# Kernel optimization log

Measured on AMD Instinct MI355X. Metric: run time of the kernel, lower is better.

The kernel has to match this reference:

```python
import jax, jax.numpy as jnp
import numpy as np

# Model dims (match init_kwargs)
M = 4          # bits per symbol
T = 32         # spike-encoding timesteps
F = 41         # input_features (tap window)
H = 256        # hidden_features
O = 16         # output_features
B = 4096       # batch

# LIF parameters (norse LIFParameters as constructed in __init__)
DT = 0.001
ALPHA = 100.0
V_TH = 1.0
V_LEAK = 0.0
V_RESET = 0.0
TAU_MEM_INV = 100.0
TAU_SYN_INV = 200.0


@jax.custom_vjp
def spike(x):
    # norse heaviside with SuperSpike surrogate gradient
    return (x > 0).astype(x.dtype)

def _spike_fwd(x):
    return spike(x), x

def _spike_bwd(x, g):
    return (g / (ALPHA * jnp.abs(x) + 1.0) ** 2,)

spike.defvjp(_spike_fwd, _spike_bwd)


def setup_inputs() -> dict:
    key = jax.random.key(0)
    ks = jax.random.split(key, 6)
    x = jax.random.randint(ks[0], (B, F), 0, 2 ** M)  # symbol indices
    # nn.Embedding default init: N(0,1)
    emb = jax.random.normal(ks[1], (2 ** M, M * T), dtype=jnp.float32)
    # nn.Linear default init: U(-1/sqrt(fan_in), 1/sqrt(fan_in))
    s_in = 1.0 / np.sqrt(M * F)
    W_in = jax.random.uniform(ks[2], (H, M * F), minval=-s_in, maxval=s_in, dtype=jnp.float32)
    W_rec = jax.random.normal(ks[3], (H, H), dtype=jnp.float32) / np.sqrt(H)
    W_rec = W_rec * (1.0 - jnp.eye(H, dtype=jnp.float32))  # autapses=False: zero diagonal
    s_out = 1.0 / np.sqrt(H)
    W_out = jax.random.uniform(ks[4], (O, H), minval=-s_out, maxval=s_out, dtype=jnp.float32)
    b_out = jax.random.uniform(ks[5], (O,), minval=-s_out, maxval=s_out, dtype=jnp.float32)
    return {"x": x, "emb": emb, "W_in": W_in, "W_rec": W_rec, "W_out": W_out, "b_out": b_out}


def reference(x, emb, W_in, W_rec, W_out, b_out):
    b = x.shape[0]
    xe = emb[x]                                      # (B, F, M*T)
    xe = xe.reshape(b, T, M * F).transpose(1, 0, 2)  # (T, B, M*F)

    z0 = jnp.zeros((b, H), jnp.float32)
    v0 = jnp.full((b, H), V_LEAK, jnp.float32)
    i0 = jnp.zeros((b, H), jnp.float32)

    def step(carry, xt):
        z, v, i = carry
        # LIF dynamics (norse lif_step): decay membrane & synaptic current
        v_dec = v + DT * TAU_MEM_INV * ((V_LEAK - v) + i)
        i_dec = i * (1.0 - DT * TAU_SYN_INV)
        z_new = spike(v_dec - V_TH)
        v_new = (1.0 - z_new) * v_dec + z_new * V_RESET
        # new current: feedforward input + recurrence on PREVIOUS spikes
        i_new = i_dec + xt @ W_in.T + z @ W_rec.T
        out_t = z_new @ W_out.T + b_out
        return (z_new, v_new, i_new), (z_new, out_t)

    _, (spikes, outs) = jax.lax.scan(step, (z0, v0, i0), xe)
    spikerate = jnp.sum(spikes) / (T * b * H)
    z_sum = jnp.sum(outs, axis=0)  # decode: sum over timesteps -> (B, O)
    return z_sum, spikerate
```

## Files before the change

kernel.cpp:

```cpp
#include <hip/hip_runtime.h>


#define T_STEPS 32
#define FDIM    41
#define HDIM    256
#define ODIM    16
#define BDIM    4096
#define MF      164

#define P_FLOATS  (32 * 3 * 16 * 256)
#define WT_FLOATS (256 * 256)

__global__ __launch_bounds__(256) void k_prep(const float* __restrict__ emb,
                                              const float* __restrict__ W_in,
                                              const float* __restrict__ W_rec,
                                              float* __restrict__ P,
                                              float* __restrict__ WT,
                                              int* __restrict__ counter)
{
    const int bid = blockIdx.x;
    const int tid = threadIdx.x;

    if (bid < 96) {
        const int t  = bid / 3;
        const int si = bid % 3;
        const int k0   = t * MF;
        const int f    = (k0 >> 7) + si;
        const int base = f << 7;
        const int c0   = max(k0, base) - base;
        const int c1   = min(k0 + MF, base + 128) - base;
        const int len  = c1 - c0;

        if (len <= 0) {
            #pragma unroll
            for (int s = 0; s < 16; ++s)
                P[((t * 3 + si) * 16 + s) * 256 + tid] = 0.0f;
            return;
        }

        __shared__ float emb_lds[16][128];
        for (int idx = tid; idx < 16 * 128; idx += 256) {
            const int s = idx >> 7, u = idx & 127;
            if (u < len) emb_lds[s][u] = emb[(s << 7) + c0 + u];
        }
        __syncthreads();

        const int j0 = base + c0 - k0;
        double acc[16];
        #pragma unroll
        for (int s = 0; s < 16; ++s) acc[s] = 0.0;
        for (int u = 0; u < len; ++u) {
            const double w = (double)W_in[tid * MF + j0 + u];
            #pragma unroll
            for (int s = 0; s < 16; ++s)
                acc[s] += w * (double)emb_lds[s][u];
        }
        #pragma unroll
        for (int s = 0; s < 16; ++s)
            P[((t * 3 + si) * 16 + s) * 256 + tid] = (float)acc[s];
    } else {
        const int h = bid - 96;
        WT[h * 256 + tid] = W_rec[tid * 256 + h];
        if (h == 0 && tid == 0) *counter = 0;
    }
}

__global__ __launch_bounds__(256) void k_main(const int* __restrict__ x,
                                              const float* __restrict__ P,
                                              const float* __restrict__ WT,
                                              const float* __restrict__ W_out,
                                              const float* __restrict__ b_out,
                                              float* __restrict__ out,
                                              int* __restrict__ counter)
{
#pragma clang fp contract(off)
    __shared__ float cnt_lds[4][256];
    __shared__ int   red[4];

    const int tid  = threadIdx.x;
    const int lane = tid & 63;
    const int wv   = __builtin_amdgcn_readfirstlane(tid >> 6);
    const int b    = blockIdx.x * 4 + wv;

    const int*    __restrict__ xb  = x + b * FDIM;
    const float4* __restrict__ P4  = (const float4*)P;
    const float4* __restrict__ WT4 = (const float4*)WT;

    int sym[FDIM];
    #pragma unroll
    for (int f = 0; f < FDIM; ++f)
        sym[f] = __builtin_amdgcn_readfirstlane(xb[f]);

    float vx = 0.f, vy = 0.f, vz = 0.f, vw = 0.f;
    float ix = 0.f, iy = 0.f, iz = 0.f, iw = 0.f;
    int   n0 = 0, n1 = 0, n2 = 0, n3 = 0;
    unsigned long long m0 = 0, m1 = 0, m2 = 0, m3 = 0;

    float4 pf[4][3];

    #define ISSUE(T, SLOT)                                                   \
        do {                                                                 \
            const int f0_ = ((T) * MF) >> 7;                                 \
            const int f2_ = (f0_ + 2 < FDIM) ? f0_ + 2 : FDIM - 1;           \
            pf[SLOT][0] = P4[(((T) * 3 + 0) * 16 + sym[f0_]) * 64 + lane];   \
            pf[SLOT][1] = P4[(((T) * 3 + 1) * 16 + sym[f0_ + 1]) * 64 + lane];\
            pf[SLOT][2] = P4[(((T) * 3 + 2) * 16 + sym[f2_]) * 64 + lane];   \
        } while (0)

    #pragma unroll
    for (int t = 0; t < 4; ++t) ISSUE(t, t);

    #pragma unroll
    for (int t = 0; t < T_STEPS; ++t) {
        const int slot = t & 3;

        const float4 p0 = pf[slot][0];
        const float4 p1 = pf[slot][1];
        const float4 p2 = pf[slot][2];

        if (t + 4 < T_STEPS) ISSUE(t + 4, slot);

        const float fx = (p0.x + p1.x) + p2.x;
        const float fy = (p0.y + p1.y) + p2.y;
        const float fz = (p0.z + p1.z) + p2.z;
        const float fw = (p0.w + p1.w) + p2.w;

        float rx = 0.f, ry = 0.f, rz = 0.f, rw = 0.f;
        while (m0) {
            const int l = __builtin_ctzll(m0); m0 &= m0 - 1;
            const float4 w = WT4[(4 * l + 0) * 64 + lane];
            rx += w.x; ry += w.y; rz += w.z; rw += w.w;
        }
        while (m1) {
            const int l = __builtin_ctzll(m1); m1 &= m1 - 1;
            const float4 w = WT4[(4 * l + 1) * 64 + lane];
            rx += w.x; ry += w.y; rz += w.z; rw += w.w;
        }
        while (m2) {
            const int l = __builtin_ctzll(m2); m2 &= m2 - 1;
            const float4 w = WT4[(4 * l + 2) * 64 + lane];
            rx += w.x; ry += w.y; rz += w.z; rw += w.w;
        }
        while (m3) {
            const int l = __builtin_ctzll(m3); m3 &= m3 - 1;
            const float4 w = WT4[(4 * l + 3) * 64 + lane];
            rx += w.x; ry += w.y; rz += w.z; rw += w.w;
        }

        const float vdx = vx + 0.1f * (ix - vx);
        const float vdy = vy + 0.1f * (iy - vy);
        const float vdz = vz + 0.1f * (iz - vz);
        const float vdw = vw + 0.1f * (iw - vw);
        const float idx_ = ix * 0.8f;
        const float idy_ = iy * 0.8f;
        const float idz_ = iz * 0.8f;
        const float idw_ = iw * 0.8f;

        const bool z0 = vdx > 1.0f;
        const bool z1 = vdy > 1.0f;
        const bool z2 = vdz > 1.0f;
        const bool z3 = vdw > 1.0f;

        vx = z0 ? 0.0f : vdx;
        vy = z1 ? 0.0f : vdy;
        vz = z2 ? 0.0f : vdz;
        vw = z3 ? 0.0f : vdw;

        ix = (idx_ + fx) + rx;
        iy = (idy_ + fy) + ry;
        iz = (idz_ + fz) + rz;
        iw = (idw_ + fw) + rw;

        n0 += z0; n1 += z1; n2 += z2; n3 += z3;

        m0 = __ballot(z0);
        m1 = __ballot(z1);
        m2 = __ballot(z2);
        m3 = __ballot(z3);
    }
    #undef ISSUE

    cnt_lds[wv][4 * lane + 0] = (float)n0;
    cnt_lds[wv][4 * lane + 1] = (float)n1;
    cnt_lds[wv][4 * lane + 2] = (float)n2;
    cnt_lds[wv][4 * lane + 3] = (float)n3;

    int myspk = n0 + n1 + n2 + n3;
    #pragma unroll
    for (int off = 32; off > 0; off >>= 1)
        myspk += __shfl_down(myspk, off, 64);
    if (lane == 0) red[wv] = myspk;

    __syncthreads();
    if (tid == 0) atomicAdd(counter, red[0] + red[1] + red[2] + red[3]);

    {
        const int o = lane & 15;
        const int q = lane >> 4;
        const float* __restrict__ wo = W_out + o * 256 + q * 64;
        const float* __restrict__ cl = cnt_lds[wv] + q * 64;
        float acc = 0.0f;
        #pragma unroll 8
        for (int h = 0; h < 64; ++h)
            acc += cl[h] * wo[h];
        acc += __shfl_down(acc, 16, 64);
        acc += __shfl_down(acc, 32, 64);
        if (q == 0)
            out[b * ODIM + o] = 32.0f * b_out[o] + acc;
    }
}

__global__ void k_fin(const int* __restrict__ counter, float* __restrict__ out)
{
    out[BDIM * ODIM] = (float)(*counter) * (1.0f / 33554432.0f);
}

extern "C" void kernel_launch(void* const* d_in, const int* in_sizes, int n_in,
                              void* d_out, int out_size, void* d_ws, size_t ws_size,
                              hipStream_t stream)
{
    const int*   x     = (const int*)  d_in[0];
    const float* emb   = (const float*)d_in[1];
    const float* W_in  = (const float*)d_in[2];
    const float* W_rec = (const float*)d_in[3];
    const float* W_out = (const float*)d_in[4];
    const float* b_out = (const float*)d_in[5];
    float* out = (float*)d_out;

    float* P       = (float*)d_ws;
    float* WT      = P + P_FLOATS;
    int*   counter = (int*)(WT + WT_FLOATS);

    k_prep<<<96 + 256, 256, 0, stream>>>(emb, W_in, W_rec, P, WT, counter);
    k_main<<<BDIM / 4, 256, 0, stream>>>(x, P, WT, W_out, b_out, out, counter);
    k_fin<<<1, 1, 0, stream>>>(counter, out);
}
```

Before: 59.12 us.

## Compact spike indices in LDS and prefetch recurrent weight rows one step ahead

The serial ctz loop over ballot masks is replaced by a compaction step: each wave writes the indices of spiking neurons into an LDS list using mbcnt prefix counts. The recurrent weight rows for up to 12 spikes are then issued as batched loads one timestep before they are needed, using A/B double-buffered register sets, and a zero-padded sentinel row in WT keeps the groups of four uniform. The aim is to overlap the dependent global loads with the LIF update and to remove the serialized load-then-add chain. The cost is much higher register pressure from the 24 float4 buffers plus extra LDS traffic, and any spikes beyond 12 still fall back to an in-step loop.

```diff
diff --git a/kernel.cpp b/kernel.cpp
--- a/kernel.cpp
+++ b/kernel.cpp
@@ -1,15 +1,23 @@
 #include <hip/hip_runtime.h>
 
+
+typedef float f32x4 __attribute__((ext_vector_type(4)));
+typedef int   i32x4 __attribute__((ext_vector_type(4)));
 
 #define T_STEPS 32
 #define FDIM    41
-#define HDIM    256
 #define ODIM    16
 #define BDIM    4096
 #define MF      164
 
 #define P_FLOATS  (32 * 3 * 16 * 256)
-#define WT_FLOATS (256 * 256)
+#define WT_ROWS   257
+#define WT_FLOATS (WT_ROWS * 256)
+
+__device__ __forceinline__ unsigned mbcnt64(unsigned long long m) {
+    unsigned lo = __builtin_amdgcn_mbcnt_lo((unsigned)m, 0u);
+    return __builtin_amdgcn_mbcnt_hi((unsigned)(m >> 32), lo);
+}
 
 __global__ __launch_bounds__(256) void k_prep(const float* __restrict__ emb,
                                               const float* __restrict__ W_in,
@@ -60,8 +68,12 @@
             P[((t * 3 + si) * 16 + s) * 256 + tid] = (float)acc[s];
     } else {
         const int h = bid - 96;
-        WT[h * 256 + tid] = W_rec[tid * 256 + h];
-        if (h == 0 && tid == 0) *counter = 0;
+        if (h < 256) {
+            WT[h * 256 + tid] = W_rec[tid * 256 + h];
+        } else {
+            WT[256 * 256 + tid] = 0.0f;
+            if (tid == 0) *counter = 0;
+        }
     }
 }
 
@@ -74,6 +86,8 @@
                                               int* __restrict__ counter)
 {
 #pragma clang fp contract(off)
+    __shared__ int   list_lds[4][256];
+    __shared__ int   xs_lds[4][48];
     __shared__ float cnt_lds[4][256];
     __shared__ int   red[4];
 
@@ -82,103 +96,111 @@
     const int wv   = __builtin_amdgcn_readfirstlane(tid >> 6);
     const int b    = blockIdx.x * 4 + wv;
 
-    const int*    __restrict__ xb  = x + b * FDIM;
-    const float4* __restrict__ P4  = (const float4*)P;
-    const float4* __restrict__ WT4 = (const float4*)WT;
-
-    int sym[FDIM];
+    const f32x4* __restrict__ P4  = (const f32x4*)P;
+    const f32x4* __restrict__ WT4 = (const f32x4*)WT;
+    int* L   = list_lds[wv];
+    int* xsL = xs_lds[wv];
+
+    if (lane < 48) xsL[lane] = (lane < FDIM) ? x[b * FDIM + lane] : 0;
+
+    f32x4 vm  = {0.f, 0.f, 0.f, 0.f};
+    f32x4 cur = {0.f, 0.f, 0.f, 0.f};
+    int n0 = 0, n1 = 0, n2 = 0, n3 = 0;
+
+    f32x4 wA[12], wB[12];
+    f32x4 pA0, pA1, pA2, pB0, pB1, pB2;
+    f32x4 rextA = {0.f, 0.f, 0.f, 0.f}, rextB;
+    int   cntA = 0, cntB;
     #pragma unroll
-    for (int f = 0; f < FDIM; ++f)
-        sym[f] = __builtin_amdgcn_readfirstlane(xb[f]);
-
-    float vx = 0.f, vy = 0.f, vz = 0.f, vw = 0.f;
-    float ix = 0.f, iy = 0.f, iz = 0.f, iw = 0.f;
-    int   n0 = 0, n1 = 0, n2 = 0, n3 = 0;
-    unsigned long long m0 = 0, m1 = 0, m2 = 0, m3 = 0;
-
-    float4 pf[4][3];
-
-    #define ISSUE(T, SLOT)                                                   \
-        do {                                                                 \
-            const int f0_ = ((T) * MF) >> 7;                                 \
-            const int f2_ = (f0_ + 2 < FDIM) ? f0_ + 2 : FDIM - 1;           \
-            pf[SLOT][0] = P4[(((T) * 3 + 0) * 16 + sym[f0_]) * 64 + lane];   \
-            pf[SLOT][1] = P4[(((T) * 3 + 1) * 16 + sym[f0_ + 1]) * 64 + lane];\
-            pf[SLOT][2] = P4[(((T) * 3 + 2) * 16 + sym[f2_]) * 64 + lane];   \
-        } while (0)
-
-    #pragma unroll
-    for (int t = 0; t < 4; ++t) ISSUE(t, t);
-
-    #pragma unroll
-    for (int t = 0; t < T_STEPS; ++t) {
-        const int slot = t & 3;
-
-        const float4 p0 = pf[slot][0];
-        const float4 p1 = pf[slot][1];
-        const float4 p2 = pf[slot][2];
-
-        if (t + 4 < T_STEPS) ISSUE(t + 4, slot);
-
-        const float fx = (p0.x + p1.x) + p2.x;
-        const float fy = (p0.y + p1.y) + p2.y;
-        const float fz = (p0.z + p1.z) + p2.z;
-        const float fw = (p0.w + p1.w) + p2.w;
-
-        float rx = 0.f, ry = 0.f, rz = 0.f, rw = 0.f;
-        while (m0) {
-            const int l = __builtin_ctzll(m0); m0 &= m0 - 1;
-            const float4 w = WT4[(4 * l + 0) * 64 + lane];
-            rx += w.x; ry += w.y; rz += w.z; rw += w.w;
-        }
-        while (m1) {
-            const int l = __builtin_ctzll(m1); m1 &= m1 - 1;
-            const float4 w = WT4[(4 * l + 1) * 64 + lane];
-            rx += w.x; ry += w.y; rz += w.z; rw += w.w;
-        }
-        while (m2) {
-            const int l = __builtin_ctzll(m2); m2 &= m2 - 1;
-            const float4 w = WT4[(4 * l + 2) * 64 + lane];
-            rx += w.x; ry += w.y; rz += w.z; rw += w.w;
-        }
-        while (m3) {
-            const int l = __builtin_ctzll(m3); m3 &= m3 - 1;
-            const float4 w = WT4[(4 * l + 3) * 64 + lane];
-            rx += w.x; ry += w.y; rz += w.z; rw += w.w;
-        }
-
-        const float vdx = vx + 0.1f * (ix - vx);
-        const float vdy = vy + 0.1f * (iy - vy);
-        const float vdz = vz + 0.1f * (iz - vz);
-        const float vdw = vw + 0.1f * (iw - vw);
-        const float idx_ = ix * 0.8f;
-        const float idy_ = iy * 0.8f;
-        const float idz_ = iz * 0.8f;
-        const float idw_ = iw * 0.8f;
-
-        const bool z0 = vdx > 1.0f;
-        const bool z1 = vdy > 1.0f;
-        const bool z2 = vdz > 1.0f;
-        const bool z3 = vdw > 1.0f;
-
-        vx = z0 ? 0.0f : vdx;
-        vy = z1 ? 0.0f : vdy;
-        vz = z2 ? 0.0f : vdz;
-        vw = z3 ? 0.0f : vdw;
-
-        ix = (idx_ + fx) + rx;
-        iy = (idy_ + fy) + ry;
-        iz = (idz_ + fz) + rz;
-        iw = (idw_ + fw) + rw;
-
-        n0 += z0; n1 += z1; n2 += z2; n3 += z3;
-
-        m0 = __ballot(z0);
-        m1 = __ballot(z1);
-        m2 = __ballot(z2);
-        m3 = __ballot(z3);
-    }
-    #undef ISSUE
+    for (int k = 0; k < 12; ++k) { wA[k] = rextA; wB[k] = rextA; }
+    pB0 = pB1 = pB2 = rextA; rextB = rextA; cntB = 0;
+
+    {
+        const int s0 = xsL[0], s1 = xsL[1], s2 = xsL[2];
+        pA0 = P4[(0 * 16 + s0) * 64 + lane];
+        pA1 = P4[(1 * 16 + s1) * 64 + lane];
+        pA2 = P4[(2 * 16 + s2) * 64 + lane];
+    }
+
+    #define STEP(TT1, ISSP, C, N)                                             \
+    {                                                                         \
+                      \
+        const f32x4 df   = cur - vm;                                          \
+        const f32x4 vdec = vm + 0.1f * df;                                    \
+        const f32x4 idec = cur * 0.8f;                                        \
+        const bool z0 = vdec.x > 1.0f, z1 = vdec.y > 1.0f,                    \
+                   z2 = vdec.z > 1.0f, z3 = vdec.w > 1.0f;                    \
+        const unsigned long long m0 = __ballot(z0), m1 = __ballot(z1),        \
+                                 m2 = __ballot(z2), m3 = __ballot(z3);        \
+        vm.x = z0 ? 0.0f : vdec.x;  vm.y = z1 ? 0.0f : vdec.y;                \
+        vm.z = z2 ? 0.0f : vdec.z;  vm.w = z3 ? 0.0f : vdec.w;                \
+        n0 += z0; n1 += z1; n2 += z2; n3 += z3;                               \
+                \
+        const f32x4 ff = (p##C##0 + p##C##1) + p##C##2;                       \
+        f32x4 rec = rext##C;                                                  \
+        if (cnt##C > 0) { rec += w##C[0];  rec += w##C[1];                    \
+                          rec += w##C[2];  rec += w##C[3]; }                  \
+        if (cnt##C > 4) { rec += w##C[4];  rec += w##C[5];                    \
+                          rec += w##C[6];  rec += w##C[7]; }                  \
+        if (cnt##C > 8) { rec += w##C[8];  rec += w##C[9];                    \
+                          rec += w##C[10]; rec += w##C[11]; }                 \
+        cur = (idec + ff) + rec;                                              \
+                                     \
+        if (ISSP) {                                                           \
+            const int f0_ = ((TT1) * MF) >> 7;                                \
+            const int s0_ = xsL[f0_], s1_ = xsL[f0_ + 1], s2_ = xsL[f0_ + 2]; \
+            p##N##0 = P4[(((TT1) * 3 + 0) * 16 + s0_) * 64 + lane];           \
+            p##N##1 = P4[(((TT1) * 3 + 1) * 16 + s1_) * 64 + lane];           \
+            p##N##2 = P4[(((TT1) * 3 + 2) * 16 + s2_) * 64 + lane];           \
+        }                                                                     \
+                    \
+        const int c0_ = __popcll(m0), c1_ = __popcll(m1),                     \
+                  c2_ = __popcll(m2), c3_ = __popcll(m3);                     \
+        const int o1_ = c0_, o2_ = o1_ + c1_, o3_ = o2_ + c2_;                \
+        cnt##N = o3_ + c3_;                                                   \
+        const unsigned r0_ = mbcnt64(m0), r1_ = mbcnt64(m1),                  \
+                       r2_ = mbcnt64(m2), r3_ = mbcnt64(m3);                  \
+        if (lane < 12) L[lane] = 256;               \
+        if (z0) L[      r0_] = 4 * lane + 0;                                  \
+        if (z1) L[o1_ + r1_] = 4 * lane + 1;                                  \
+        if (z2) L[o2_ + r2_] = 4 * lane + 2;                                  \
+        if (z3) L[o3_ + r3_] = 4 * lane + 3;                                  \
+        rext##N = (f32x4){0.f, 0.f, 0.f, 0.f};                                \
+        if (cnt##N > 0) {                                                     \
+            const i32x4 u = *(const i32x4*)&L[0];                             \
+            w##N[0] = WT4[u.x * 64 + lane]; w##N[1] = WT4[u.y * 64 + lane];   \
+            w##N[2] = WT4[u.z * 64 + lane]; w##N[3] = WT4[u.w * 64 + lane];   \
+        }                                                                     \
+        if (cnt##N > 4) {                                                     \
+            const i32x4 u = *(const i32x4*)&L[4];                             \
+            w##N[4] = WT4[u.x * 64 + lane]; w##N[5] = WT4[u.y * 64 + lane];   \
+            w##N[6] = WT4[u.z * 64 + lane]; w##N[7] = WT4[u.w * 64 + lane];   \
+        }                                                                     \
+        if (cnt##N > 8) {                                                     \
+            const i32x4 u = *(const i32x4*)&L[8];                             \
+            w##N[8]  = WT4[u.x * 64 + lane]; w##N[9]  = WT4[u.y * 64 + lane]; \
+            w##N[10] = WT4[u.z * 64 + lane]; w##N[11] = WT4[u.w * 64 + lane]; \
+        }                                                                     \
+        if (cnt##N > 12) {                   \
+            int k_ = 12;                                                      \
+            for (; k_ + 3 < cnt##N; k_ += 4) {                                \
+                const i32x4 u = *(const i32x4*)&L[k_];                        \
+                const f32x4 a0 = WT4[u.x * 64 + lane];                        \
+                const f32x4 a1 = WT4[u.y * 64 + lane];                        \
+                const f32x4 a2 = WT4[u.z * 64 + lane];                        \
+                const f32x4 a3 = WT4[u.w * 64 + lane];                        \
+                rext##N += ((a0 + a1) + (a2 + a3));                           \
+            }                                                                 \
+            for (; k_ < cnt##N; ++k_)                                         \
+                rext##N += WT4[L[k_] * 64 + lane];                            \
+        }                                                                     \
+    }
+
+    for (int tt = 0; tt < T_STEPS; tt += 2) {
+        STEP(tt + 1, 1, A, B);
+        STEP(tt + 2, (tt + 2 < T_STEPS), B, A);
+    }
+    #undef STEP
 
     cnt_lds[wv][4 * lane + 0] = (float)n0;
     cnt_lds[wv][4 * lane + 1] = (float)n1;
@@ -231,7 +253,7 @@
     float* WT      = P + P_FLOATS;
     int*   counter = (int*)(WT + WT_FLOATS);
 
-    k_prep<<<96 + 256, 256, 0, stream>>>(emb, W_in, W_rec, P, WT, counter);
+    k_prep<<<96 + 257, 256, 0, stream>>>(emb, W_in, W_rec, P, WT, counter);
     k_main<<<BDIM / 4, 256, 0, stream>>>(x, P, WT, W_out, b_out, out, counter);
     k_fin<<<1, 1, 0, stream>>>(counter, out);
 }
```

After: 73.95 us. +25.1%, slower.
